# Kernel optimization log

Measured on AMD Instinct MI355X. Metric: run time of the kernel, lower is better.

## Reference

```python
import jax, jax.numpy as jnp
import numpy as np

DT = 0.1
EPS = 0.01


def _trans_layer(x, W, b):
    # x: [B, 2U]; W: [U, U]; b: [U]
    U = b.shape[0]
    t = DT / EPS
    u_in, v_in = x[:, :U], x[:, U:]
    act = jnp.tanh(u_in)
    v_star = (v_in + t * act) / (1.0 + t)
    # Block matrix A = [[I, dt*W], [-dt*W^T, I]] -- identical for all samples,
    # so factor/solve ONCE with a multi-RHS solve instead of torch's per-sample batched LU.
    I = jnp.eye(U, dtype=x.dtype)
    A = jnp.block([[I, DT * W], [-DT * W.T, I]])  # [2U, 2U]
    rhs = jnp.concatenate([u_in + DT * b, v_star], axis=1)  # [B, 2U]
    y = jnp.linalg.solve(A, rhs.T).T  # [B, 2U]
    u, v = y[:, :U], y[:, U:]
    u_out = DT * (v @ W.T) - u_in - DT * b
    v_out = -DT * (u @ W) + t * v - v_in - t * act
    return jnp.concatenate([u_out, v_out], axis=1)


def setup_inputs() -> dict:
    key = jax.random.key(0)
    ks = jax.random.split(key, 14)
    B, D_IN, U, D_OUT = 32768, 256, 256, 10

    def lin_w(k, o, i):
        return (jax.random.uniform(k, (o, i), jnp.float32) * 2.0 - 1.0) / np.sqrt(i).astype(np.float32)

    def lin_b(k, o, fan_in):
        return (jax.random.uniform(k, (o,), jnp.float32) * 2.0 - 1.0) / np.sqrt(fan_in).astype(np.float32)

    return {
        'x': jax.random.normal(ks[0], (B, D_IN), jnp.float32),
        'Wi': lin_w(ks[1], U, D_IN), 'bi': lin_b(ks[2], U, D_IN),
        'W1': lin_w(ks[3], U, U), 'b1': lin_b(ks[4], U, U),
        'W2': lin_w(ks[5], U, U), 'b2': lin_b(ks[6], U, U),
        'W3': lin_w(ks[7], U, U), 'b3': lin_b(ks[8], U, U),
        'W4': lin_w(ks[9], U, U), 'b4': lin_b(ks[10], U, U),
        'Wo': lin_w(ks[11], D_OUT, U), 'bo': lin_b(ks[12], D_OUT, U),
    }


def reference(x, Wi, bi, W1, b1, W2, b2, W3, b3, W4, b4, Wo, bo):
    U = W1.shape[0]
    z = x @ Wi.T + bi                       # linearInput
    z = jnp.concatenate([z, jnp.tanh(z)], axis=1)  # [B, 2U]
    for W, b in ((W1, b1), (W2, b2), (W3, b3), (W4, b4)):
        z = _trans_layer(z, W, b)
    z = z[:, :U]
    logits = z @ Wo.T + bo                  # linearOutput
    return jax.nn.softmax(logits, axis=1)
```

## Files before the change

### kernel.cpp

```cpp
#include <hip/hip_runtime.h>
#include <math.h>

#define DTC 0.1f

typedef _Float16 half8 __attribute__((ext_vector_type(8)));
typedef _Float16 half4v __attribute__((ext_vector_type(4)));
typedef float f32x4 __attribute__((ext_vector_type(4)));
typedef float f32x2 __attribute__((ext_vector_type(2)));

__device__ __forceinline__ float fast_tanh(float x) {
  const float e = __expf(2.f * x);
  const float r = __builtin_amdgcn_rcpf(e + 1.f);
  return fmaf(-2.f, r, 1.f);
}


__global__ __launch_bounds__(256) void k_prep(
    const float* __restrict__ W0, const float* __restrict__ W1,
    const float* __restrict__ W2, const float* __restrict__ W3,
    const float* __restrict__ b2, const float* __restrict__ b3,
    const float* __restrict__ b4,
    _Float16* __restrict__ Wh, _Float16* __restrict__ Wt,
    float* __restrict__ crm) {
  const float* Ws[4] = {W0, W1, W2, W3};
  const int bid = blockIdx.x, tid = threadIdx.x;
  if (bid < 128) {
    const int t = bid * 256 + tid;
    const float* W = Ws[(t * 8) >> 16];
    const int off = (t * 8) & 65535;
    const float4 a = *(const float4*)&W[off];
    const float4 b = *(const float4*)&W[off + 4];
    half8 h;
    h[0] = (_Float16)a.x; h[1] = (_Float16)a.y; h[2] = (_Float16)a.z; h[3] = (_Float16)a.w;
    h[4] = (_Float16)b.x; h[5] = (_Float16)b.y; h[6] = (_Float16)b.z; h[7] = (_Float16)b.w;
    *(half8*)&Wh[t * 8] = h;
  } else if (bid < 384) {
    __shared__ float sh[32][33];
    const int b2i = bid - 128;
    const int l = b2i >> 6, t64 = b2i & 63;
    const int r0 = (t64 >> 3) * 32, c0 = (t64 & 7) * 32;
    const float* W = Ws[l];
    const int i = tid >> 5, j = tid & 31;
#pragma unroll
    for (int p = 0; p < 4; ++p)
      sh[p * 8 + i][j] = W[(r0 + p * 8 + i) * 256 + c0 + j];
    __syncthreads();
#pragma unroll
    for (int p = 0; p < 4; ++p)
      Wt[l * 65536 + (c0 + p * 8 + i) * 256 + r0 + j] = (_Float16)sh[j][p * 8 + i];
  } else {
    const int l = bid - 384;
    const float* W = Ws[l];
    const float* b = (l == 0) ? b2 : (l == 1) ? b3 : b4;
    float s = 0.f;
#pragma unroll 8
    for (int k = 0; k < 256; ++k) s = fmaf(b[k], W[k * 256 + tid], s);
    crm[l * 256 + tid] = -0.09f * s;
  }
}

__global__ __launch_bounds__(256) void k_smm3(const _Float16* __restrict__ A,
                                              const _Float16* __restrict__ B,
                                              const _Float16* __restrict__ Eadd,
                                              _Float16* __restrict__ C,
                                              float scale, int addI) {
  const int tid = threadIdx.x, wave = tid >> 6, lane = tid & 63;
  const int quad = lane >> 4, l16 = lane & 15;
  const int l = blockIdx.z;
  const _Float16* Al = A + (size_t)l * 65536;
  const _Float16* Bl = B + (size_t)l * 65536;
  _Float16* Cl = C + (size_t)l * 65536;
  const int m0 = blockIdx.y * 64 + wave * 16, n0 = blockIdx.x * 64;
  f32x4 acc[4] = {};
#pragma unroll
  for (int kt = 0; kt < 8; ++kt) {
    const half8 af = *(const half8*)&Al[(m0 + l16) * 256 + kt * 32 + quad * 8];
#pragma unroll
    for (int ni = 0; ni < 4; ++ni) {
      const half8 bf = *(const half8*)&Bl[(n0 + ni * 16 + l16) * 256 + kt * 32 + quad * 8];
      acc[ni] = __builtin_amdgcn_mfma_f32_16x16x32_f16(af, bf, acc[ni], 0, 0, 0);
    }
  }
#pragma unroll
  for (int ni = 0; ni < 4; ++ni)
#pragma unroll
    for (int r = 0; r < 4; ++r) {
      const int row = m0 + quad * 4 + r, col = n0 + ni * 16 + l16;
      float v = scale * acc[ni][r];
      if (addI) v += (row == col ? 1.f : 0.f) - (float)(Eadd + (size_t)l * 65536)[row * 256 + col];
      Cl[row * 256 + col] = (_Float16)v;
    }
}

__global__ __launch_bounds__(256) void k_pack(
    const _Float16* __restrict__ Ph, const _Float16* __restrict__ Qt,
    const _Float16* __restrict__ Wt, const float* __restrict__ Wi,
    const float* __restrict__ Wo,
    _Float16* __restrict__ PQP, _Float16* __restrict__ RmP,
    _Float16* __restrict__ WiP, _Float16* __restrict__ WoP) {
  const int t = blockIdx.x * 256 + threadIdx.x;
  if (t < 65536) {
    const int l = t >> 14, c = t & 16383;
    const int ntile = c >> 10, kt = (c >> 6) & 15, lb = c & 63;
    const int n = ntile * 16 + (lb & 15);
    const int kq = (lb >> 4) * 8;
    half8 h;
    if (kt < 8) {
      h = *(const half8*)&Ph[(size_t)l * 65536 + n * 256 + kt * 32 + kq];
#pragma unroll
      for (int j = 0; j < 8; ++j) h[j] = -h[j];
    } else {
      h = *(const half8*)&Qt[(size_t)l * 65536 + n * 256 + (kt - 8) * 32 + kq];
    }
    *(half8*)&PQP[(size_t)t * 8] = h;
  } else if (t < 90112) {
    const int tt = t - 65536;
    const int l = tt >> 13, c = tt & 8191;
    const int ntile = c >> 9, kt = (c >> 6) & 7, lb = c & 63;
    const int n = ntile * 16 + (lb & 15);
    const int k0 = kt * 32 + (lb >> 4) * 8;
    half8 h = *(const half8*)&Wt[(size_t)l * 65536 + n * 256 + k0];
#pragma unroll
    for (int j = 0; j < 8; ++j) h[j] = (_Float16)(-0.9f * (float)h[j]);
    *(half8*)&RmP[(size_t)tt * 8] = h;
  } else if (t < 98304) {
    const int c = t - 90112;
    const int ntile = c >> 9, kt = (c >> 6) & 7, lb = c & 63;
    const int n = ntile * 16 + (lb & 15);
    const int k0 = kt * 32 + (lb >> 4) * 8;
    const float4 a = *(const float4*)&Wi[n * 256 + k0];
    const float4 b = *(const float4*)&Wi[n * 256 + k0 + 4];
    half8 h;
    h[0] = (_Float16)a.x; h[1] = (_Float16)a.y; h[2] = (_Float16)a.z; h[3] = (_Float16)a.w;
    h[4] = (_Float16)b.x; h[5] = (_Float16)b.y; h[6] = (_Float16)b.z; h[7] = (_Float16)b.w;
    *(half8*)&WiP[(size_t)c * 8] = h;
  } else {
    const int c = t - 98304;
    const int kt = c >> 6, lb = c & 63;
    const int n = lb & 15;
    const int k0 = kt * 32 + (lb >> 4) * 8;
    half8 h;
#pragma unroll
    for (int j = 0; j < 8; ++j) h[j] = (_Float16)((n < 10) ? Wo[n * 256 + k0 + j] : 0.f);
    *(half8*)&WoP[(size_t)c * 8] = h;
  }
}



template <int NKT, bool DUAL>
__device__ __forceinline__ void gemm_k(const _Float16* __restrict__ Bp,
                                       const _Float16* A1, const _Float16* A2,
                                       f32x4* acc, int wave, int lane, int quad, int l16) {
  half8 bf[4][2];
  auto loadB = [&](int kt, int s) {
#pragma unroll
    for (int ni = 0; ni < 2; ++ni)
      bf[s][ni] = *(const half8*)&Bp[(((wave * 2 + ni) * NKT + kt) * 64 + lane) * 8];
  };
  loadB(0, 0);
  loadB(1, 1);
  loadB(2, 2);
  const char* a1b = (const char*)A1 + lane * 16;
  const char* a2b = (const char*)A2 + lane * 16;
#pragma unroll
  for (int kt = 0; kt < NKT; ++kt) {
    const int s = kt & 3;
    if (kt + 3 < NKT) loadB(kt + 3, (kt + 3) & 3);
    const char* Ab = (DUAL && kt >= NKT / 2) ? a2b : a1b;
    const int akt = DUAL ? (kt & (NKT / 2 - 1)) : kt;
    half8 af[4];
#pragma unroll
    for (int mi = 0; mi < 4; ++mi)
      af[mi] = *(const half8*)(Ab + (akt * 4 + mi) * 1024);
    __builtin_amdgcn_s_setprio(1);
#pragma unroll
    for (int mi = 0; mi < 4; ++mi)
#pragma unroll
      for (int ni = 0; ni < 2; ++ni)
        acc[mi * 2 + ni] = __builtin_amdgcn_mfma_f32_16x16x32_f16(
            bf[s][ni], af[mi], acc[mi * 2 + ni], 0, 0, 0);
    __builtin_amdgcn_s_setprio(0);
  }
}

__global__ __launch_bounds__(512, 2) void k_fused(
    const float* __restrict__ x, const _Float16* __restrict__ WiP,
    const _Float16* __restrict__ PQP, const _Float16* __restrict__ RmP,
    const _Float16* __restrict__ WoP, const float* __restrict__ bi,
    const float* __restrict__ b1, const float* __restrict__ b2,
    const float* __restrict__ b3, const float* __restrict__ b4,
    const float* __restrict__ crm, const float* __restrict__ bo,
    float* __restrict__ out) {
  __shared__ __align__(16) _Float16 A1[64 * 256];
  __shared__ __align__(16) _Float16 A2[64 * 256];
  const int tid = threadIdx.x;
  const int wave = tid >> 6, lane = tid & 63;
  const int quad = lane >> 4, l16 = lane & 15;
  const int m0 = blockIdx.x * 64;

#pragma unroll
  for (int mi = 0; mi < 4; ++mi) {
    const size_t gb = (size_t)(m0 + mi * 16 + l16) * 256 + wave * 32 + quad * 8;
    const float4 a = *(const float4*)&x[gb];
    const float4 b = *(const float4*)&x[gb + 4];
    half8 h;
    h[0] = (_Float16)a.x; h[1] = (_Float16)a.y; h[2] = (_Float16)a.z; h[3] = (_Float16)a.w;
    h[4] = (_Float16)b.x; h[5] = (_Float16)b.y; h[6] = (_Float16)b.z; h[7] = (_Float16)b.w;
    *(half8*)((char*)A1 + ((wave * 4 + mi) * 64 + lane) * 16) = h;
  }
  __syncthreads();

  f32x4 acc[8];
  const f32x4 zero = {0.f, 0.f, 0.f, 0.f};
  half4v uph[8], r2p[8];

  char* e1 = (char*)A1 + wave * 4096 + ((quad >> 1) * 16 + l16) * 16 + (quad & 1) * 8;
  char* e2 = (char*)A2 + wave * 4096 + ((quad >> 1) * 16 + l16) * 16 + (quad & 1) * 8;

#pragma unroll
  for (int t = 0; t < 8; ++t) acc[t] = zero;
  gemm_k<8, false>(WiP, A1, A1, acc, wave, lane, quad, l16);
  __syncthreads();
#pragma unroll
  for (int ni = 0; ni < 2; ++ni) {
    const int col0 = wave * 32 + ni * 16 + quad * 4;
    const f32x4 bi4 = *(const f32x4*)&bi[col0];
    const f32x4 b14 = *(const f32x4*)&b1[col0];
#pragma unroll
    for (int mi = 0; mi < 4; ++mi) {
      const int off = mi * 1024 + ni * 512;
      half4v h1, h2;
#pragma unroll
      for (int r = 0; r < 4; ++r) {
        const float z = acc[mi * 2 + ni][r] + bi4[r];
        h1[r] = (_Float16)(z + DTC * b14[r]);
        h2[r] = (_Float16)fast_tanh(z);
      }
      *(half4v*)(e1 + off) = h1;
      *(half4v*)(e2 + off) = h2;
      r2p[mi * 2 + ni] = h2;
    }
  }
  __syncthreads();

#pragma unroll 1
  for (int l = 0; l < 4; ++l) {
#pragma unroll
    for (int t = 0; t < 8; ++t) acc[t] = zero;
    gemm_k<16, true>(PQP + (size_t)l * 131072, A1, A2, acc, wave, lane, quad, l16);
    __syncthreads();
    const float* bn = (l == 0) ? b2 : (l == 1) ? b3 : b4;
#pragma unroll
    for (int ni = 0; ni < 2; ++ni) {
      const int col0 = wave * 32 + ni * 16 + quad * 4;
      f32x4 bn4 = zero;
      if (l < 3) bn4 = DTC * (*(const f32x4*)&bn[col0]);
#pragma unroll
      for (int mi = 0; mi < 4; ++mi) {
        const int off = mi * 1024 + ni * 512;
        half4v hu, h1;
#pragma unroll
        for (int r = 0; r < 4; ++r) {
          const float u = acc[mi * 2 + ni][r];
          hu[r] = (_Float16)u;
          h1[r] = (_Float16)(u + bn4[r]);
        }
        uph[mi * 2 + ni] = hu;
        *(half4v*)(e1 + off) = h1;
      }
    }
    __syncthreads();
    if (l < 3) {
#pragma unroll
      for (int t = 0; t < 8; ++t) acc[t] = zero;
      gemm_k<8, false>(RmP + (size_t)l * 65536, A1, A1, acc, wave, lane, quad, l16);
#pragma unroll
      for (int ni = 0; ni < 2; ++ni) {
        const int col0 = wave * 32 + ni * 16 + quad * 4;
        const f32x4 cc4 = *(const f32x4*)&crm[l * 256 + col0];
#pragma unroll
        for (int mi = 0; mi < 4; ++mi) {
          const int off = mi * 1024 + ni * 512;
          half4v nr2;
#pragma unroll
          for (int r = 0; r < 4; ++r) {
            const float vp = acc[mi * 2 + ni][r] - cc4[r] - (float)r2p[mi * 2 + ni][r];
            nr2[r] = (_Float16)((vp + 10.f * fast_tanh((float)uph[mi * 2 + ni][r])) * (1.f / 11.f));
          }
          r2p[mi * 2 + ni] = nr2;
          *(half4v*)(e2 + off) = nr2;
        }
      }
      __syncthreads();
    }
  }

  if (wave < 4) {
    f32x4 acch = zero;
#pragma unroll
    for (int kt = 0; kt < 8; ++kt) {
      const half8 af = *(const half8*)((const char*)A1 +
                                       ((kt * 4 + wave) * 64 + lane) * 16);
      const half8 bfr = *(const half8*)&WoP[(kt * 64 + lane) * 8];
      acch = __builtin_amdgcn_mfma_f32_16x16x32_f16(bfr, af, acch, 0, 0, 0);
    }
    float v4[4];
    float mx = -3.0e38f;
#pragma unroll
    for (int r = 0; r < 4; ++r) {
      const int cls = quad * 4 + r;
      const float v = acch[r] + ((cls < 10) ? bo[cls] : -3.0e38f);
      v4[r] = v;
      mx = fmaxf(mx, v);
    }
    mx = fmaxf(mx, __shfl_xor(mx, 16, 64));
    mx = fmaxf(mx, __shfl_xor(mx, 32, 64));
    float e4[4], s = 0.f;
#pragma unroll
    for (int r = 0; r < 4; ++r) {
      e4[r] = __expf(v4[r] - mx);
      s += e4[r];
    }
    s += __shfl_xor(s, 16, 64);
    s += __shfl_xor(s, 32, 64);
    const float rs = __builtin_amdgcn_rcpf(s);
    float* op = &out[(size_t)(m0 + wave * 16 + l16) * 10 + quad * 4];
    if (quad < 2) {
      f32x2 p0 = {e4[0] * rs, e4[1] * rs};
      f32x2 p1 = {e4[2] * rs, e4[3] * rs};
      *(f32x2*)op = p0;
      *(f32x2*)(op + 2) = p1;
    } else if (quad == 2) {
      f32x2 p0 = {e4[0] * rs, e4[1] * rs};
      *(f32x2*)op = p0;
    }
  }
}


extern "C" void kernel_launch(void* const* d_in, const int* in_sizes, int n_in,
                              void* d_out, int out_size, void* d_ws, size_t ws_size,
                              hipStream_t stream) {
  const float* x  = (const float*)d_in[0];
  const float* Wi = (const float*)d_in[1];
  const float* bi = (const float*)d_in[2];
  const float* W[4] = {(const float*)d_in[3], (const float*)d_in[5],
                       (const float*)d_in[7], (const float*)d_in[9]};
  const float* b[4] = {(const float*)d_in[4], (const float*)d_in[6],
                       (const float*)d_in[8], (const float*)d_in[10]};
  const float* Wo = (const float*)d_in[11];
  const float* bo = (const float*)d_in[12];
  float* out = (float*)d_out;

  const int Bsz = in_sizes[0] / 256;

  _Float16* hb = (_Float16*)d_ws;
  _Float16* WiP = hb;
  _Float16* WoP = hb + 65536;
  _Float16* PQP = hb + 69632;
  _Float16* RmP = hb + 593920;
  _Float16* Wh  = hb + 790528;
  _Float16* Wt  = hb + 1052672;
  _Float16* Eh  = hb + 1314816;
  _Float16* Ph  = hb + 1576960;
  _Float16* Qt  = hb + 1839104;
  float* crm = (float*)(hb + 2101248);

  const dim3 g64(4, 4, 4);
  k_prep<<<387, 256, 0, stream>>>(W[0], W[1], W[2], W[3], b[1], b[2], b[3],
                                  Wh, Wt, crm);
  k_smm3<<<g64, 256, 0, stream>>>(Wh, Wh, nullptr, Eh, 0.01f, 0);
  k_smm3<<<g64, 256, 0, stream>>>(Eh, Eh, Eh, Ph, 1.0f, 1);
  k_smm3<<<g64, 256, 0, stream>>>(Ph, Wt, nullptr, Qt, DTC, 0);
  k_pack<<<386, 256, 0, stream>>>(Ph, Qt, Wt, Wi, Wo, PQP, RmP, WiP, WoP);

  k_fused<<<Bsz / 64, 512, 0, stream>>>(x, WiP, PQP, RmP, WoP, bi,
                                        b[0], b[1], b[2], b[3], crm, bo, out);
}
```

Baseline: 186.4 us.

## Use 4-wave blocks with 64-column wave tiles in fused kernel

Result: no change. 183.0 us (-1.8%).

```diff
diff --git a/kernel.cpp b/kernel.cpp
--- a/kernel.cpp
+++ b/kernel.cpp
@@ -151,12 +151,12 @@
 template <int NKT, bool DUAL>
 __device__ __forceinline__ void gemm_k(const _Float16* __restrict__ Bp,
                                        const _Float16* A1, const _Float16* A2,
-                                       f32x4* acc, int wave, int lane, int quad, int l16) {
-  half8 bf[4][2];
+                                       f32x4* acc, int wave, int lane) {
+  half8 bf[4][4];
   auto loadB = [&](int kt, int s) {
 #pragma unroll
-    for (int ni = 0; ni < 2; ++ni)
-      bf[s][ni] = *(const half8*)&Bp[(((wave * 2 + ni) * NKT + kt) * 64 + lane) * 8];
+    for (int ni = 0; ni < 4; ++ni)
+      bf[s][ni] = *(const half8*)&Bp[(((wave * 4 + ni) * NKT + kt) * 64 + lane) * 8];
   };
   loadB(0, 0);
   loadB(1, 1);
@@ -177,14 +177,14 @@
 #pragma unroll
     for (int mi = 0; mi < 4; ++mi)
 #pragma unroll
-      for (int ni = 0; ni < 2; ++ni)
-        acc[mi * 2 + ni] = __builtin_amdgcn_mfma_f32_16x16x32_f16(
-            bf[s][ni], af[mi], acc[mi * 2 + ni], 0, 0, 0);
+      for (int ni = 0; ni < 4; ++ni)
+        acc[mi * 4 + ni] = __builtin_amdgcn_mfma_f32_16x16x32_f16(
+            bf[s][ni], af[mi], acc[mi * 4 + ni], 0, 0, 0);
     __builtin_amdgcn_s_setprio(0);
   }
 }
 
-__global__ __launch_bounds__(512, 2) void k_fused(
+__global__ __launch_bounds__(256, 2) void k_fused(
     const float* __restrict__ x, const _Float16* __restrict__ WiP,
     const _Float16* __restrict__ PQP, const _Float16* __restrict__ RmP,
     const _Float16* __restrict__ WoP, const float* __restrict__ bi,
@@ -200,46 +200,50 @@
   const int m0 = blockIdx.x * 64;
 
 #pragma unroll
-  for (int mi = 0; mi < 4; ++mi) {
-    const size_t gb = (size_t)(m0 + mi * 16 + l16) * 256 + wave * 32 + quad * 8;
-    const float4 a = *(const float4*)&x[gb];
-    const float4 b = *(const float4*)&x[gb + 4];
-    half8 h;
-    h[0] = (_Float16)a.x; h[1] = (_Float16)a.y; h[2] = (_Float16)a.z; h[3] = (_Float16)a.w;
-    h[4] = (_Float16)b.x; h[5] = (_Float16)b.y; h[6] = (_Float16)b.z; h[7] = (_Float16)b.w;
-    *(half8*)((char*)A1 + ((wave * 4 + mi) * 64 + lane) * 16) = h;
+  for (int kk = 0; kk < 2; ++kk) {
+    const int kt = wave + kk * 4;
+#pragma unroll
+    for (int mi = 0; mi < 4; ++mi) {
+      const size_t gb = (size_t)(m0 + mi * 16 + l16) * 256 + kt * 32 + quad * 8;
+      const float4 a = *(const float4*)&x[gb];
+      const float4 b = *(const float4*)&x[gb + 4];
+      half8 h;
+      h[0] = (_Float16)a.x; h[1] = (_Float16)a.y; h[2] = (_Float16)a.z; h[3] = (_Float16)a.w;
+      h[4] = (_Float16)b.x; h[5] = (_Float16)b.y; h[6] = (_Float16)b.z; h[7] = (_Float16)b.w;
+      *(half8*)((char*)A1 + ((kt * 4 + mi) * 64 + lane) * 16) = h;
+    }
   }
   __syncthreads();
 
-  f32x4 acc[8];
+  f32x4 acc[16];
   const f32x4 zero = {0.f, 0.f, 0.f, 0.f};
-  half4v uph[8], r2p[8];
-
-  char* e1 = (char*)A1 + wave * 4096 + ((quad >> 1) * 16 + l16) * 16 + (quad & 1) * 8;
-  char* e2 = (char*)A2 + wave * 4096 + ((quad >> 1) * 16 + l16) * 16 + (quad & 1) * 8;
-
-#pragma unroll
-  for (int t = 0; t < 8; ++t) acc[t] = zero;
-  gemm_k<8, false>(WiP, A1, A1, acc, wave, lane, quad, l16);
+  half4v uph[16];
+
+  const int ebase = wave * 8192 + (quad >> 1) * 256 + l16 * 16 + (quad & 1) * 8;
+  char* e1 = (char*)A1 + ebase;
+  char* e2 = (char*)A2 + ebase;
+
+#pragma unroll
+  for (int t = 0; t < 16; ++t) acc[t] = zero;
+  gemm_k<8, false>(WiP, A1, A1, acc, wave, lane);
   __syncthreads();
 #pragma unroll
-  for (int ni = 0; ni < 2; ++ni) {
-    const int col0 = wave * 32 + ni * 16 + quad * 4;
+  for (int ni = 0; ni < 4; ++ni) {
+    const int col0 = wave * 64 + ni * 16 + quad * 4;
     const f32x4 bi4 = *(const f32x4*)&bi[col0];
     const f32x4 b14 = *(const f32x4*)&b1[col0];
 #pragma unroll
     for (int mi = 0; mi < 4; ++mi) {
-      const int off = mi * 1024 + ni * 512;
+      const int off = (ni >> 1) * 4096 + mi * 1024 + (ni & 1) * 512;
       half4v h1, h2;
 #pragma unroll
       for (int r = 0; r < 4; ++r) {
-        const float z = acc[mi * 2 + ni][r] + bi4[r];
+        const float z = acc[mi * 4 + ni][r] + bi4[r];
         h1[r] = (_Float16)(z + DTC * b14[r]);
         h2[r] = (_Float16)fast_tanh(z);
       }
       *(half4v*)(e1 + off) = h1;
       *(half4v*)(e2 + off) = h2;
-      r2p[mi * 2 + ni] = h2;
     }
   }
   __syncthreads();
@@ -247,48 +251,48 @@
 #pragma unroll 1
   for (int l = 0; l < 4; ++l) {
 #pragma unroll
-    for (int t = 0; t < 8; ++t) acc[t] = zero;
-    gemm_k<16, true>(PQP + (size_t)l * 131072, A1, A2, acc, wave, lane, quad, l16);
+    for (int t = 0; t < 16; ++t) acc[t] = zero;
+    gemm_k<16, true>(PQP + (size_t)l * 131072, A1, A2, acc, wave, lane);
     __syncthreads();
     const float* bn = (l == 0) ? b2 : (l == 1) ? b3 : b4;
 #pragma unroll
-    for (int ni = 0; ni < 2; ++ni) {
-      const int col0 = wave * 32 + ni * 16 + quad * 4;
+    for (int ni = 0; ni < 4; ++ni) {
+      const int col0 = wave * 64 + ni * 16 + quad * 4;
       f32x4 bn4 = zero;
       if (l < 3) bn4 = DTC * (*(const f32x4*)&bn[col0]);
 #pragma unroll
       for (int mi = 0; mi < 4; ++mi) {
-        const int off = mi * 1024 + ni * 512;
+        const int off = (ni >> 1) * 4096 + mi * 1024 + (ni & 1) * 512;
         half4v hu, h1;
 #pragma unroll
         for (int r = 0; r < 4; ++r) {
-          const float u = acc[mi * 2 + ni][r];
+          const float u = acc[mi * 4 + ni][r];
           hu[r] = (_Float16)u;
           h1[r] = (_Float16)(u + bn4[r]);
         }
-        uph[mi * 2 + ni] = hu;
+        uph[mi * 4 + ni] = hu;
         *(half4v*)(e1 + off) = h1;
       }
     }
     __syncthreads();
     if (l < 3) {
 #pragma unroll
-      for (int t = 0; t < 8; ++t) acc[t] = zero;
-      gemm_k<8, false>(RmP + (size_t)l * 65536, A1, A1, acc, wave, lane, quad, l16);
-#pragma unroll
-      for (int ni = 0; ni < 2; ++ni) {
-        const int col0 = wave * 32 + ni * 16 + quad * 4;
+      for (int t = 0; t < 16; ++t) acc[t] = zero;
+      gemm_k<8, false>(RmP + (size_t)l * 65536, A1, A1, acc, wave, lane);
+#pragma unroll
+      for (int ni = 0; ni < 4; ++ni) {
+        const int col0 = wave * 64 + ni * 16 + quad * 4;
         const f32x4 cc4 = *(const f32x4*)&crm[l * 256 + col0];
 #pragma unroll
         for (int mi = 0; mi < 4; ++mi) {
-          const int off = mi * 1024 + ni * 512;
+          const int off = (ni >> 1) * 4096 + mi * 1024 + (ni & 1) * 512;
+          const half4v r2o = *(const half4v*)(e2 + off);
           half4v nr2;
 #pragma unroll
           for (int r = 0; r < 4; ++r) {
-            const float vp = acc[mi * 2 + ni][r] - cc4[r] - (float)r2p[mi * 2 + ni][r];
-            nr2[r] = (_Float16)((vp + 10.f * fast_tanh((float)uph[mi * 2 + ni][r])) * (1.f / 11.f));
+            const float vp = acc[mi * 4 + ni][r] - cc4[r] - (float)r2o[r];
+            nr2[r] = (_Float16)((vp + 10.f * fast_tanh((float)uph[mi * 4 + ni][r])) * (1.f / 11.f));
           }
-          r2p[mi * 2 + ni] = nr2;
           *(half4v*)(e2 + off) = nr2;
         }
       }
@@ -296,7 +300,7 @@
     }
   }
 
-  if (wave < 4) {
+  {
     f32x4 acch = zero;
 #pragma unroll
     for (int kt = 0; kt < 8; ++kt) {
@@ -375,6 +379,6 @@
   k_smm3<<<g64, 256, 0, stream>>>(Ph, Wt, nullptr, Qt, DTC, 0);
   k_pack<<<386, 256, 0, stream>>>(Ph, Qt, Wt, Wi, Wo, PQP, RmP, WiP, WoP);
 
-  k_fused<<<Bsz / 64, 512, 0, stream>>>(x, WiP, PQP, RmP, WoP, bi,
+  k_fused<<<Bsz / 64, 256, 0, stream>>>(x, WiP, PQP, RmP, WoP, bi,
                                         b[0], b[1], b[2], b[3], crm, bo, out);
 }
```
